# Performance work log

Hardware: AMD Instinct MI355X
Metric: run time of the kernel (lower is better)

## Reference

```python
import jax, jax.numpy as jnp
import numpy as np

L = 6          # n_layers
T = 256        # seq_len
B = 32         # batch
N = 1024       # n_features (factor_dim)
H = 16         # n_heads
HD = 64        # head_dim
PD = H * HD    # packed_dim_size == N here
FF = 4096      # dim_feedforward
EPS = 1e-5


def setup_inputs() -> dict:
    key = jax.random.key(0)
    ks = jax.random.split(key, 6)
    s = 0.02  # weight init scale (xavier-ish for these dims)
    return {
        "src": jax.random.normal(ks[0], (T, B, N), jnp.float32),
        "attn_mask": jnp.zeros((T, T), jnp.float32),  # additive mask
        "Wqkv": jax.random.normal(ks[1], (L, 3 * PD, N), jnp.float32) * s,
        "bqkv": jnp.zeros((L, 3 * PD), jnp.float32),
        "Wo": jax.random.normal(ks[2], (L, N, PD), jnp.float32) * s,
        "bo": jnp.zeros((L, N), jnp.float32),
        "ln1_g": jnp.ones((L, N), jnp.float32),
        "ln1_b": jnp.zeros((L, N), jnp.float32),
        "ln2_g": jnp.ones((L, N), jnp.float32),
        "ln2_b": jnp.zeros((L, N), jnp.float32),
        "W1": jax.random.normal(ks[3], (L, FF, N), jnp.float32) * s,
        "b1": jnp.zeros((L, FF), jnp.float32),
        "W2": jax.random.normal(ks[4], (L, N, FF), jnp.float32) * s,
        "b2": jnp.zeros((L, N), jnp.float32),
        "lnf_g": jnp.ones((N,), jnp.float32),
        "lnf_b": jnp.zeros((N,), jnp.float32),
    }


def _layer_norm(x, g, b):
    m = x.mean(-1, keepdims=True)
    v = ((x - m) ** 2).mean(-1, keepdims=True)
    return (x - m) * jax.lax.rsqrt(v + EPS) * g + b


def reference(src, attn_mask, Wqkv, bqkv, Wo, bo, ln1_g, ln1_b, ln2_g, ln2_b,
              W1, b1, W2, b2, lnf_g, lnf_b):
    inv_sqrt_hd = 1.0 / np.sqrt(HD).astype(np.float32)

    def layer(x, p):
        wqkv, bq, wo, bo_, g1, bb1n, g2, bb2n, w1, bb1, w2, bb2 = p
        # --- self-attention block (pre-norm) ---
        h = _layer_norm(x, g1, bb1n)                       # [T,B,N]
        qkv = jnp.einsum('tbn,pn->tbp', h, wqkv) + bq      # [T,B,3*PD]
        q, k, v = jnp.split(qkv, 3, axis=-1)
        q = q.reshape(T, B, H, HD) * inv_sqrt_hd
        k = k.reshape(T, B, H, HD)
        v = v.reshape(T, B, H, HD)
        scores = jnp.einsum('tbhd,sbhd->bhts', q, k) + attn_mask  # [B,H,T,T]
        probs = jax.nn.softmax(scores, axis=-1)
        o = jnp.einsum('bhts,sbhd->tbhd', probs, v).reshape(T, B, PD)
        x = x + jnp.einsum('tbp,np->tbn', o, wo) + bo_
        # --- FFN block (pre-norm) ---
        h = _layer_norm(x, g2, bb2n)
        ff = jax.nn.relu(jnp.einsum('tbn,fn->tbf', h, w1) + bb1)
        x = x + jnp.einsum('tbf,nf->tbn', ff, w2) + bb2
        return x, None

    params = (Wqkv, bqkv, Wo, bo, ln1_g, ln1_b, ln2_g, ln2_b, W1, b1, W2, b2)
    x, _ = jax.lax.scan(layer, src, params)
    return _layer_norm(x, lnf_g, lnf_b)
```

## Files before the change

kernel.cpp:

```cpp
#include <hip/hip_runtime.h>
#include <math.h>

#define TS 256
#define BS 32
#define NF 1024
#define NH 16
#define HD 64
#define PD 1024
#define FFD 4096
#define NLAYER 6
#define ROWS (TS*BS)
#define LNEPS 1e-5f

typedef unsigned int u32;
typedef __attribute__((ext_vector_type(8))) short bf16x8;
typedef __attribute__((ext_vector_type(4))) float f32x4;

__device__ __forceinline__ unsigned short f2bf(float f) {
    u32 u = __builtin_bit_cast(u32, f);
    u32 r = (u + 0x7fffu + ((u >> 16) & 1u)) >> 16;
    return (unsigned short)r;
}

__device__ __forceinline__ void async16(const void* g, void* l) {
    __builtin_amdgcn_global_load_lds(
        (const __attribute__((address_space(1))) u32*)g,
        (__attribute__((address_space(3))) u32*)l, 16, 0, 0);
}

template <int BF16OUT>
__global__ __launch_bounds__(256)
void ln_kernel(const float* __restrict__ x, void* __restrict__ y,
               const float* __restrict__ g, const float* __restrict__ b) {
    int row = blockIdx.x;
    int tid = threadIdx.x;
    const float4* xr = (const float4*)(x + (size_t)row * NF);
    float4 v = xr[tid];
    float s  = v.x + v.y + v.z + v.w;
    float ss = v.x*v.x + v.y*v.y + v.z*v.z + v.w*v.w;
    #pragma unroll
    for (int off = 32; off > 0; off >>= 1) {
        s  += __shfl_down(s,  off);
        ss += __shfl_down(ss, off);
    }
    __shared__ float ws[4], wss[4];
    int wid = tid >> 6, lane = tid & 63;
    if (lane == 0) { ws[wid] = s; wss[wid] = ss; }
    __syncthreads();
    float sum   = ws[0] + ws[1] + ws[2] + ws[3];
    float sumsq = wss[0] + wss[1] + wss[2] + wss[3];
    float mean = sum * (1.0f / NF);
    float var  = sumsq * (1.0f / NF) - mean * mean;
    float rstd = rsqrtf(var + LNEPS);
    float4 gv = ((const float4*)g)[tid];
    float4 bv = ((const float4*)b)[tid];
    float4 o;
    o.x = (v.x - mean) * rstd * gv.x + bv.x;
    o.y = (v.y - mean) * rstd * gv.y + bv.y;
    o.z = (v.z - mean) * rstd * gv.z + bv.z;
    o.w = (v.w - mean) * rstd * gv.w + bv.w;
    if (BF16OUT) {
        ushort4 ov;
        ov.x = f2bf(o.x); ov.y = f2bf(o.y); ov.z = f2bf(o.z); ov.w = f2bf(o.w);
        ((ushort4*)((unsigned short*)y + (size_t)row * NF))[tid] = ov;
    } else {
        ((float4*)((float*)y + (size_t)row * NF))[tid] = o;
    }
}

__global__ __launch_bounds__(256)
void f2bf4_kernel(const float* __restrict__ s0, const float* __restrict__ s1,
                  const float* __restrict__ s2, const float* __restrict__ s3,
                  unsigned short* __restrict__ d0, unsigned short* __restrict__ d1,
                  unsigned short* __restrict__ d2, unsigned short* __restrict__ d3,
                  int n0, int n1, int n2, int n3) {
    const float* s; unsigned short* d; int n;
    switch (blockIdx.y) {
        case 0: s = s0; d = d0; n = n0; break;
        case 1: s = s1; d = d1; n = n1; break;
        case 2: s = s2; d = d2; n = n2; break;
        default: s = s3; d = d3; n = n3; break;
    }
    int i = (blockIdx.x * 256 + threadIdx.x) * 4;
    if (i >= n) return;
    float4 v = *(const float4*)(s + i);
    ushort4 o;
    o.x = f2bf(v.x); o.y = f2bf(v.y); o.z = f2bf(v.z); o.w = f2bf(v.w);
    *(ushort4*)(d + i) = o;
}

template <int MODE, int RESID>
__global__ __launch_bounds__(256)
void gemm_mfma(const unsigned short* __restrict__ A, const unsigned short* __restrict__ B,
               const float* __restrict__ bias, const float* __restrict__ resid,
               void* __restrict__ Cout, int M, int N, int K) {
    __shared__ __align__(16) unsigned short sA0[128 * 64];
    __shared__ __align__(16) unsigned short sA1[128 * 64];
    __shared__ __align__(16) unsigned short sB0[128 * 64];
    __shared__ __align__(16) unsigned short sB1[128 * 64];
    int tid = threadIdx.x;

    int Nb = N >> 7;
    int bid = blockIdx.x;
    int group = bid / (8 * Nb);
    int rem = bid - group * (8 * Nb);
    int m0 = (group * 8 + rem / Nb) * 128;
    int n0 = (rem % Nb) * 128;

    int rB = tid >> 3;
    int c0 = (tid & 7) ^ (rB & 7);
    const unsigned short* gA[4];
    const unsigned short* gB[4];
    #pragma unroll
    for (int it = 0; it < 4; it++) {
        gA[it] = A + (size_t)(m0 + rB + 32 * it) * K + c0 * 8;
        gB[it] = B + (size_t)(n0 + rB + 32 * it) * K + c0 * 8;
    }

    int wid = tid >> 6, lane = tid & 63;
    int wm = wid >> 1, wn = wid & 1;
    int quad = lane >> 4, rl = lane & 15;

    int aoff[2][4], boff[2][4];
    #pragma unroll
    for (int ks = 0; ks < 2; ks++)
        #pragma unroll
        for (int t = 0; t < 4; t++) {
            int r = wm * 64 + t * 16 + rl;
            aoff[ks][t] = r * 64 + ((ks * 4 + quad) ^ (r & 7)) * 8;
            int rn = wn * 64 + t * 16 + rl;
            boff[ks][t] = rn * 64 + ((ks * 4 + quad) ^ (rn & 7)) * 8;
        }

    f32x4 acc[4][4] = {};

    auto stage = [&](int t, unsigned short* dA, unsigned short* dB) {
        int kt = t << 6;
        #pragma unroll
        for (int it = 0; it < 4; it++) {
            async16(gA[it] + kt, dA + (tid + 256 * it) * 8);
            async16(gB[it] + kt, dB + (tid + 256 * it) * 8);
        }
    };
    auto compute = [&](const unsigned short* pA, const unsigned short* pB) {
        #pragma unroll
        for (int ks = 0; ks < 2; ks++) {
            bf16x8 a[4], b[4];
            #pragma unroll
            for (int t = 0; t < 4; t++) {
                a[t] = *(const bf16x8*)(pA + aoff[ks][t]);
                b[t] = *(const bf16x8*)(pB + boff[ks][t]);
            }
            #pragma unroll
            for (int i = 0; i < 4; i++)
                #pragma unroll
                for (int j = 0; j < 4; j++)
                    acc[i][j] = __builtin_amdgcn_mfma_f32_16x16x32_bf16(a[i], b[j], acc[i][j], 0, 0, 0);
        }
    };

    int nT = K >> 6;
    stage(0, sA0, sB0);
    for (int t = 0; t < nT; t += 2) {
        __syncthreads();
        stage(t + 1, sA1, sB1);
        compute(sA0, sB0);
        __syncthreads();
        if (t + 2 < nT) stage(t + 2, sA0, sB0);
        compute(sA1, sB1);
    }

    float bvv[4];
    #pragma unroll
    for (int nt = 0; nt < 4; nt++) bvv[nt] = bias[n0 + wn * 64 + nt * 16 + rl];
    #pragma unroll
    for (int mt = 0; mt < 4; mt++) {
        #pragma unroll
        for (int nt = 0; nt < 4; nt++) {
            #pragma unroll
            for (int r = 0; r < 4; r++) {
                int row = m0 + wm * 64 + mt * 16 + quad * 4 + r;
                int col = n0 + wn * 64 + nt * 16 + rl;
                float v = acc[mt][nt][r] + bvv[nt];
                if (MODE == 0) {
                    if (RESID) v += resid[(size_t)row * N + col];
                    ((float*)Cout)[(size_t)row * N + col] = v;
                } else if (MODE == 1) {
                    v = fmaxf(v, 0.0f);
                    ((unsigned short*)Cout)[(size_t)row * N + col] = f2bf(v);
                } else {
                    int t = row >> 5, bb = row & 31;
                    int s = col >> 10, hh = (col >> 6) & 15, d = col & 63;
                    if (s == 0) v *= 0.125f;
                    ((unsigned short*)Cout)[((((size_t)s * BS + bb) * NH + hh) * TS + t) * HD + d] = f2bf(v);
                }
            }
        }
    }
}

__global__ __launch_bounds__(256, 2)
void attn_mfma(const unsigned short* __restrict__ qkvT, const float* __restrict__ mask,
               unsigned short* __restrict__ o) {
    int bx = blockIdx.x;
    int bh = bx >> 1, half = bx & 1;
    int b = bh >> 4, h = bh & 15;
    const unsigned short* qB = qkvT + (size_t)bh * TS * HD;
    const unsigned short* kB = qB + (size_t)BS * NH * TS * HD;
    const unsigned short* vB = kB + (size_t)BS * NH * TS * HD;
    int tid = threadIdx.x, lane = tid & 63, wid = tid >> 6;
    int quad = lane >> 4, rl = lane & 15;
    int tbase = half * 128 + wid * 32;

    __shared__ __align__(16) unsigned short sKV[18432];
    __shared__ __align__(16) unsigned short sP[4][1280];

    #pragma unroll
    for (int it = 0; it < 8; it++) {
        int idx = it * 256 + tid, rrow = idx >> 3, ch = idx & 7;
        *(uint4*)(sKV + rrow * 72 + ch * 8) = *(const uint4*)(kB + (size_t)rrow * 64 + ch * 8);
    }

    bf16x8 qf[2][2];
    #pragma unroll
    for (int mt = 0; mt < 2; mt++)
        #pragma unroll
        for (int ks = 0; ks < 2; ks++)
            qf[mt][ks] = *(const bf16x8*)(qB + (size_t)(tbase + mt * 16 + rl) * 64 + ks * 32 + quad * 8);

    __syncthreads();

    f32x4 S[2][16] = {};
    #pragma unroll
    for (int nt = 0; nt < 16; nt++) {
        bf16x8 k0 = *(const bf16x8*)(sKV + (nt * 16 + rl) * 72 + quad * 8);
        bf16x8 k1 = *(const bf16x8*)(sKV + (nt * 16 + rl) * 72 + 32 + quad * 8);
        #pragma unroll
        for (int mt = 0; mt < 2; mt++) {
            S[mt][nt] = __builtin_amdgcn_mfma_f32_16x16x32_bf16(qf[mt][0], k0, S[mt][nt], 0, 0, 0);
            S[mt][nt] = __builtin_amdgcn_mfma_f32_16x16x32_bf16(qf[mt][1], k1, S[mt][nt], 0, 0, 0);
        }
    }

    float linv[2][4];
    #pragma unroll
    for (int mt = 0; mt < 2; mt++) {
        #pragma unroll
        for (int r = 0; r < 4; r++) {
            int tg = tbase + mt * 16 + quad * 4 + r;
            const float* mrow = mask + (size_t)tg * TS + rl;
            float mx = -3.0e38f;
            #pragma unroll
            for (int nt = 0; nt < 16; nt++) {
                S[mt][nt][r] += mrow[nt * 16];
                mx = fmaxf(mx, S[mt][nt][r]);
            }
            mx = fmaxf(mx, __shfl_xor(mx, 1));
            mx = fmaxf(mx, __shfl_xor(mx, 2));
            mx = fmaxf(mx, __shfl_xor(mx, 4));
            mx = fmaxf(mx, __shfl_xor(mx, 8));
            float sum = 0.0f;
            #pragma unroll
            for (int nt = 0; nt < 16; nt++) {
                float p = __expf(S[mt][nt][r] - mx);
                S[mt][nt][r] = p;
                sum += p;
            }
            sum += __shfl_xor(sum, 1);
            sum += __shfl_xor(sum, 2);
            sum += __shfl_xor(sum, 4);
            sum += __shfl_xor(sum, 8);
            linv[mt][r] = 1.0f / sum;
        }
    }

    __syncthreads();
    #pragma unroll
    for (int it = 0; it < 8; it++) {
        int idx = it * 256 + tid, srow = idx >> 3, dc = idx & 7;
        bf16x8 vv = *(const bf16x8*)(vB + (size_t)srow * 64 + dc * 8);
        #pragma unroll
        for (int j = 0; j < 8; j++)
            sKV[(dc * 8 + j) * 264 + srow] = (unsigned short)vv[j];
    }
    __syncthreads();

    f32x4 O[2][4] = {};
    unsigned short* myP = sP[wid];
    #pragma unroll
    for (int sc = 0; sc < 8; sc++) {
        #pragma unroll
        for (int mt = 0; mt < 2; mt++)
            #pragma unroll
            for (int hi = 0; hi < 2; hi++)
                #pragma unroll
                for (int r = 0; r < 4; r++)
                    myP[(mt * 16 + quad * 4 + r) * 40 + hi * 16 + rl] = f2bf(S[mt][2 * sc + hi][r]);
        bf16x8 pa[2], vf[4];
        #pragma unroll
        for (int mt = 0; mt < 2; mt++)
            pa[mt] = *(const bf16x8*)(myP + (mt * 16 + rl) * 40 + quad * 8);
        #pragma unroll
        for (int nd = 0; nd < 4; nd++)
            vf[nd] = *(const bf16x8*)(sKV + (nd * 16 + rl) * 264 + sc * 32 + quad * 8);
        #pragma unroll
        for (int mt = 0; mt < 2; mt++)
            #pragma unroll
            for (int nd = 0; nd < 4; nd++)
                O[mt][nd] = __builtin_amdgcn_mfma_f32_16x16x32_bf16(pa[mt], vf[nd], O[mt][nd], 0, 0, 0);
    }

    #pragma unroll
    for (int mt = 0; mt < 2; mt++)
        #pragma unroll
        for (int nd = 0; nd < 4; nd++)
            #pragma unroll
            for (int r = 0; r < 4; r++) {
                int tg = tbase + mt * 16 + quad * 4 + r;
                int d = nd * 16 + rl;
                o[(size_t)(tg * BS + b) * PD + h * HD + d] = f2bf(O[mt][nd][r] * linv[mt][r]);
            }
}

extern "C" void kernel_launch(void* const* d_in, const int* in_sizes, int n_in,
                              void* d_out, int out_size, void* d_ws, size_t ws_size,
                              hipStream_t stream) {
    const float* src  = (const float*)d_in[0];
    const float* mask = (const float*)d_in[1];
    const float* Wqkv = (const float*)d_in[2];
    const float* bqkv = (const float*)d_in[3];
    const float* Wo   = (const float*)d_in[4];
    const float* bo   = (const float*)d_in[5];
    const float* ln1g = (const float*)d_in[6];
    const float* ln1b = (const float*)d_in[7];
    const float* ln2g = (const float*)d_in[8];
    const float* ln2b = (const float*)d_in[9];
    const float* W1   = (const float*)d_in[10];
    const float* b1   = (const float*)d_in[11];
    const float* W2   = (const float*)d_in[12];
    const float* b2   = (const float*)d_in[13];
    const float* lnfg = (const float*)d_in[14];
    const float* lnfb = (const float*)d_in[15];

    float* x = (float*)d_out;
    char* ws = (char*)d_ws;
    unsigned short* qkvT = (unsigned short*)ws;
    unsigned short* ff   = (unsigned short*)ws;
    unsigned short* h    = (unsigned short*)(ws + 67108864);
    unsigned short* o    = (unsigned short*)(ws + 83886080);
    unsigned short* wbuf = (unsigned short*)(ws + 100663296);
    unsigned short* wq = wbuf;
    unsigned short* wo = wbuf + 3145728;
    unsigned short* w1 = wbuf + 4194304;
    unsigned short* w2 = wbuf + 8388608;

    hipMemcpyAsync(x, src, (size_t)ROWS * NF * 4, hipMemcpyDeviceToDevice, stream);

    for (int l = 0; l < NLAYER; l++) {
        const float* wqkv_l = Wqkv + (size_t)l * 3 * PD * NF;
        const float* bqkv_l = bqkv + (size_t)l * 3 * PD;
        const float* wo_l   = Wo + (size_t)l * NF * PD;
        const float* bo_l   = bo + (size_t)l * NF;
        const float* w1_l   = W1 + (size_t)l * FFD * NF;
        const float* b1_l   = b1 + (size_t)l * FFD;
        const float* w2_l   = W2 + (size_t)l * NF * FFD;
        const float* b2_l   = b2 + (size_t)l * NF;

        f2bf4_kernel<<<dim3(4096, 4), 256, 0, stream>>>(
            wqkv_l, wo_l, w1_l, w2_l, wq, wo, w1, w2,
            3 * PD * NF, NF * PD, FFD * NF, NF * FFD);
        ln_kernel<1><<<ROWS, 256, 0, stream>>>(x, h, ln1g + (size_t)l * NF, ln1b + (size_t)l * NF);
        gemm_mfma<2, 0><<<(ROWS / 128) * (3 * PD / 128), 256, 0, stream>>>(
            h, wq, bqkv_l, nullptr, qkvT, ROWS, 3 * PD, NF);
        attn_mfma<<<BS * NH * 2, 256, 0, stream>>>(qkvT, mask, o);
        gemm_mfma<0, 1><<<(ROWS / 128) * (NF / 128), 256, 0, stream>>>(
            o, wo, bo_l, x, x, ROWS, NF, PD);
        ln_kernel<1><<<ROWS, 256, 0, stream>>>(x, h, ln2g + (size_t)l * NF, ln2b + (size_t)l * NF);
        gemm_mfma<1, 0><<<(ROWS / 128) * (FFD / 128), 256, 0, stream>>>(
            h, w1, b1_l, nullptr, ff, ROWS, FFD, NF);
        gemm_mfma<0, 1><<<(ROWS / 128) * (NF / 128), 256, 0, stream>>>(
            ff, w2, b2_l, x, x, ROWS, NF, FFD);
    }
    ln_kernel<0><<<ROWS, 256, 0, stream>>>(x, x, lnfg, lnfb);
}
```

Measured before the change: 2.169 ms.

## Add 256x256-tile 8-wave pipelined GEMM for QKV and FFN1 projections

Adds a new bf16 MFMA GEMM kernel with 256x256 output tiles, 512 threads, double-buffered async LDS staging interleaved with four MFMA phases, XOR-swizzled LDS layout, s_setprio, and an XCD-aware block remapping. It replaces the 128x128 GEMM for the QKV projection and the first FFN projection, aiming to raise arithmetic intensity and overlap global loads with MFMA. The large tile cuts the block count (384 and 512 blocks) and uses 128 KB LDS per block, which may limit occupancy and wave balance.

```diff
diff --git a/kernel.cpp b/kernel.cpp
--- a/kernel.cpp
+++ b/kernel.cpp
@@ -199,6 +199,194 @@
     }
 }
 
+template <int MODE>
+__global__ __launch_bounds__(512, 2)
+void gemm256(const unsigned short* __restrict__ A, const unsigned short* __restrict__ B,
+             const float* __restrict__ bias, void* __restrict__ Cout,
+             int M, int N, int K) {
+    __shared__ __align__(16) unsigned short sA[2 * 256 * 64];
+    __shared__ __align__(16) unsigned short sB[2 * 256 * 64];
+    int tid = threadIdx.x;
+    (void)M;
+
+    int Nb = N >> 8;
+    int nwg = gridDim.x;
+    int bid = blockIdx.x;
+    int wgid = (bid & 7) * (nwg >> 3) + (bid >> 3);
+    int gsz = 8 * Nb;
+    int group = wgid / gsz, rem = wgid - group * gsz;
+    int m0 = (group * 8 + rem / Nb) << 8;
+    int n0 = (rem - (rem / Nb) * Nb) << 8;
+
+    int rr = tid >> 3;
+    int cd = (tid & 7) ^ (rr & 7);
+    const unsigned short* gA0 = A + (size_t)(m0 + rr) * K + cd * 8;
+    const unsigned short* gB0 = B + (size_t)(n0 + rr) * K + cd * 8;
+    size_t sK64 = (size_t)64 * K;
+
+    auto stgA = [&](int buf, int h, int kt) {
+        unsigned short* d = sA + buf * 16384 + h * 8192 + tid * 8;
+        const unsigned short* g = gA0 + (size_t)(h * 2) * sK64 + kt;
+        async16(g, d);
+        async16(g + sK64, d + 4096);
+    };
+    auto stgB = [&](int buf, int h, int kt) {
+        unsigned short* d = sB + buf * 16384 + h * 8192 + tid * 8;
+        const unsigned short* g = gB0 + (size_t)(h * 2) * sK64 + kt;
+        async16(g, d);
+        async16(g + sK64, d + 4096);
+    };
+
+    int wid = tid >> 6, lane = tid & 63;
+    int wm = wid >> 2, wn = wid & 3;
+    int quad = lane >> 4, rl = lane & 15;
+
+    int aoff[4][2], boff[4][2];
+    #pragma unroll
+    for (int j = 0; j < 4; ++j)
+        #pragma unroll
+        for (int ks = 0; ks < 2; ++ks) {
+            int r = j * 32 + wm * 16 + rl;
+            aoff[j][ks] = r * 64 + (((ks * 4 + quad) ^ (r & 7)) << 3);
+            int rn = wn * 64 + j * 16 + rl;
+            boff[j][ks] = rn * 64 + (((ks * 4 + quad) ^ (rn & 7)) << 3);
+        }
+
+    f32x4 acc[8][4] = {};
+    int nT = K >> 6;
+
+    stgA(0, 0, 0); stgB(0, 0, 0); stgA(0, 1, 0); stgB(0, 1, 0);
+    if (nT > 1) {
+        stgA(1, 0, 64); stgB(1, 0, 64); stgA(1, 1, 64);
+        asm volatile("s_waitcnt vmcnt(6)" ::: "memory");
+    } else {
+        asm volatile("s_waitcnt vmcnt(0)" ::: "memory");
+    }
+    __builtin_amdgcn_s_barrier();
+    __builtin_amdgcn_sched_barrier(0);
+
+    bf16x8 a[4][2], b[4][2];
+    for (int t = 0; t < nT; ++t) {
+        int buf = t & 1;
+        const unsigned short* pA = sA + buf * 16384;
+        const unsigned short* pB = sB + buf * 16384;
+        int kt1 = (t + 1) << 6, kt2 = (t + 2) << 6;
+        int s1 = (t + 1) < nT, s2 = (t + 2) < nT;
+
+        #pragma unroll
+        for (int j = 0; j < 4; ++j) {
+            a[j][0] = *(const bf16x8*)(pA + aoff[j][0]);
+            a[j][1] = *(const bf16x8*)(pA + aoff[j][1]);
+        }
+        #pragma unroll
+        for (int i = 0; i < 2; ++i) {
+            b[i][0] = *(const bf16x8*)(pB + boff[i][0]);
+            b[i][1] = *(const bf16x8*)(pB + boff[i][1]);
+        }
+        if (s1) stgB(buf ^ 1, 1, kt1);
+        asm volatile("s_waitcnt lgkmcnt(8)" ::: "memory");
+        __builtin_amdgcn_s_barrier();
+        asm volatile("s_waitcnt lgkmcnt(0)" ::: "memory");
+        __builtin_amdgcn_sched_barrier(0);
+        __builtin_amdgcn_s_setprio(1);
+        #pragma unroll
+        for (int j = 0; j < 4; ++j)
+            #pragma unroll
+            for (int i = 0; i < 2; ++i) {
+                acc[j][i] = __builtin_amdgcn_mfma_f32_16x16x32_bf16(a[j][0], b[i][0], acc[j][i], 0, 0, 0);
+                acc[j][i] = __builtin_amdgcn_mfma_f32_16x16x32_bf16(a[j][1], b[i][1], acc[j][i], 0, 0, 0);
+            }
+        __builtin_amdgcn_s_setprio(0);
+        __builtin_amdgcn_s_barrier();
+        __builtin_amdgcn_sched_barrier(0);
+
+        #pragma unroll
+        for (int i = 2; i < 4; ++i) {
+            b[i][0] = *(const bf16x8*)(pB + boff[i][0]);
+            b[i][1] = *(const bf16x8*)(pB + boff[i][1]);
+        }
+        if (s2) stgA(buf, 0, kt2);
+        __builtin_amdgcn_s_barrier();
+        asm volatile("s_waitcnt lgkmcnt(0)" ::: "memory");
+        __builtin_amdgcn_sched_barrier(0);
+        __builtin_amdgcn_s_setprio(1);
+        #pragma unroll
+        for (int j = 0; j < 4; ++j)
+            #pragma unroll
+            for (int i = 2; i < 4; ++i) {
+                acc[j][i] = __builtin_amdgcn_mfma_f32_16x16x32_bf16(a[j][0], b[i][0], acc[j][i], 0, 0, 0);
+                acc[j][i] = __builtin_amdgcn_mfma_f32_16x16x32_bf16(a[j][1], b[i][1], acc[j][i], 0, 0, 0);
+            }
+        __builtin_amdgcn_s_setprio(0);
+        __builtin_amdgcn_s_barrier();
+        __builtin_amdgcn_sched_barrier(0);
+
+        #pragma unroll
+        for (int j = 0; j < 4; ++j) {
+            a[j][0] = *(const bf16x8*)(pA + 8192 + aoff[j][0]);
+            a[j][1] = *(const bf16x8*)(pA + 8192 + aoff[j][1]);
+        }
+        if (s2) stgB(buf, 0, kt2);
+        __builtin_amdgcn_s_barrier();
+        asm volatile("s_waitcnt lgkmcnt(0)" ::: "memory");
+        __builtin_amdgcn_sched_barrier(0);
+        __builtin_amdgcn_s_setprio(1);
+        #pragma unroll
+        for (int j = 0; j < 4; ++j)
+            #pragma unroll
+            for (int i = 2; i < 4; ++i) {
+                acc[4 + j][i] = __builtin_amdgcn_mfma_f32_16x16x32_bf16(a[j][0], b[i][0], acc[4 + j][i], 0, 0, 0);
+                acc[4 + j][i] = __builtin_amdgcn_mfma_f32_16x16x32_bf16(a[j][1], b[i][1], acc[4 + j][i], 0, 0, 0);
+            }
+        __builtin_amdgcn_s_setprio(0);
+        __builtin_amdgcn_s_barrier();
+        __builtin_amdgcn_sched_barrier(0);
+
+        if (s2) stgA(buf, 1, kt2);
+        __builtin_amdgcn_s_barrier();
+        asm volatile("s_waitcnt lgkmcnt(0)" ::: "memory");
+        __builtin_amdgcn_sched_barrier(0);
+        __builtin_amdgcn_s_setprio(1);
+        #pragma unroll
+        for (int j = 0; j < 4; ++j)
+            #pragma unroll
+            for (int i = 0; i < 2; ++i) {
+                acc[4 + j][i] = __builtin_amdgcn_mfma_f32_16x16x32_bf16(a[j][0], b[i][0], acc[4 + j][i], 0, 0, 0);
+                acc[4 + j][i] = __builtin_amdgcn_mfma_f32_16x16x32_bf16(a[j][1], b[i][1], acc[4 + j][i], 0, 0, 0);
+            }
+        __builtin_amdgcn_s_setprio(0);
+        if (s2) asm volatile("s_waitcnt vmcnt(6)" ::: "memory");
+        else    asm volatile("s_waitcnt vmcnt(0)" ::: "memory");
+        __builtin_amdgcn_s_barrier();
+        __builtin_amdgcn_sched_barrier(0);
+    }
+
+    float bvv[4];
+    #pragma unroll
+    for (int ni = 0; ni < 4; ++ni) bvv[ni] = bias[n0 + wn * 64 + ni * 16 + rl];
+    #pragma unroll
+    for (int mi = 0; mi < 8; ++mi) {
+        #pragma unroll
+        for (int ni = 0; ni < 4; ++ni) {
+            #pragma unroll
+            for (int r = 0; r < 4; ++r) {
+                int row = m0 + mi * 32 + wm * 16 + quad * 4 + r;
+                int col = n0 + wn * 64 + ni * 16 + rl;
+                float v = acc[mi][ni][r] + bvv[ni];
+                if (MODE == 1) {
+                    v = fmaxf(v, 0.0f);
+                    ((unsigned short*)Cout)[(size_t)row * N + col] = f2bf(v);
+                } else {
+                    int tt = row >> 5, bb = row & 31;
+                    int s = col >> 10, hh = (col >> 6) & 15, d = col & 63;
+                    if (s == 0) v *= 0.125f;
+                    ((unsigned short*)Cout)[((((size_t)s * BS + bb) * NH + hh) * TS + tt) * HD + d] = f2bf(v);
+                }
+            }
+        }
+    }
+}
+
 __global__ __launch_bounds__(256, 2)
 void attn_mfma(const unsigned short* __restrict__ qkvT, const float* __restrict__ mask,
                unsigned short* __restrict__ o) {
@@ -370,14 +558,14 @@
             wqkv_l, wo_l, w1_l, w2_l, wq, wo, w1, w2,
             3 * PD * NF, NF * PD, FFD * NF, NF * FFD);
         ln_kernel<1><<<ROWS, 256, 0, stream>>>(x, h, ln1g + (size_t)l * NF, ln1b + (size_t)l * NF);
-        gemm_mfma<2, 0><<<(ROWS / 128) * (3 * PD / 128), 256, 0, stream>>>(
-            h, wq, bqkv_l, nullptr, qkvT, ROWS, 3 * PD, NF);
+        gemm256<2><<<(ROWS / 256) * (3 * PD / 256), 512, 0, stream>>>(
+            h, wq, bqkv_l, qkvT, ROWS, 3 * PD, NF);
         attn_mfma<<<BS * NH * 2, 256, 0, stream>>>(qkvT, mask, o);
         gemm_mfma<0, 1><<<(ROWS / 128) * (NF / 128), 256, 0, stream>>>(
             o, wo, bo_l, x, x, ROWS, NF, PD);
         ln_kernel<1><<<ROWS, 256, 0, stream>>>(x, h, ln2g + (size_t)l * NF, ln2b + (size_t)l * NF);
-        gemm_mfma<1, 0><<<(ROWS / 128) * (FFD / 128), 256, 0, stream>>>(
-            h, w1, b1_l, nullptr, ff, ROWS, FFD, NF);
+        gemm256<1><<<(ROWS / 256) * (FFD / 256), 512, 0, stream>>>(
+            h, w1, b1_l, ff, ROWS, FFD, NF);
         gemm_mfma<0, 1><<<(ROWS / 128) * (NF / 128), 256, 0, stream>>>(
             ff, w2, b2_l, x, x, ROWS, NF, FFD);
     }
```

After: 2.153 ms. No clear change (-0.7%).
